# Optimization experiments

Hardware: AMD Instinct MI355X
Metric: run time of the kernel (lower is better)

The kernel has to match this reference:

```python
import jax, jax.numpy as jnp
import numpy as np

NEG = -1e9


def setup_inputs() -> dict:
    key = jax.random.key(0)
    kq, kk, kv, ke = jax.random.split(key, 4)
    B, H, S, D = 4, 16, 2048, 64
    q = jax.random.normal(kq, (B, H, S, D), dtype=jnp.float32)
    k = jax.random.normal(kk, (B, H, S, D), dtype=jnp.float32)
    v = jax.random.normal(kv, (B, H, S, D), dtype=jnp.float32)
    event_length = jax.random.randint(ke, (B,), 0, S, dtype=jnp.int32)
    return {"q": q, "k": k, "v": v, "event_length": event_length}


def reference(q, k, v, event_length):
    B, H, S, D = q.shape
    scale = jnp.sqrt(jnp.asarray(D, dtype=jnp.float32))
    # [b,h,s,q] scores
    scores = jnp.einsum('bhsd,bhqd->bhsq', q, k) / scale
    idx = jnp.arange(S)
    el = event_length[:, None]  # [B,1]
    valid = idx[None, :] < el   # [B,S]
    # mask[b,s,q] = valid[b,s] & valid[b,q]; broadcast over heads
    mask = (valid[:, None, :, None] & valid[:, None, None, :])  # [B,1,S,S]
    scores = jnp.where(mask, scores, NEG)
    attn = jax.nn.softmax(scores, axis=-1)
    # dropout p=0.0 (eval): identity
    out = jnp.einsum('bhsq,bhqd->bhsd', attn, v)
    return out
```

## Files before the change

### kernel.cpp

```cpp
#include <hip/hip_runtime.h>


#define SQ 2048
#define DH 64
#define NBH 64
#define TK 64
#define LDE 72

typedef __attribute__((ext_vector_type(4))) float f32x4;
typedef __attribute__((ext_vector_type(8))) short bf16x8;
typedef __attribute__((ext_vector_type(4))) unsigned int u32x4;
typedef __attribute__((ext_vector_type(2))) unsigned int u32x2;

__device__ __forceinline__ unsigned short bf16r(float x) {
    union { float f; unsigned int u; } t; t.f = x;
    unsigned int r = t.u + 0x7fffu + ((t.u >> 16) & 1u);
    return (unsigned short)(r >> 16);
}
__device__ __forceinline__ unsigned int bf16pk(float lo, float hi) {
    return (unsigned int)bf16r(lo) | ((unsigned int)bf16r(hi) << 16);
}

__global__ __launch_bounds__(256)
void meanv_k(const float* __restrict__ V, float* __restrict__ MV) {
    const int bh  = blockIdx.x >> 4;
    const int seg = blockIdx.x & 15;
    const float* vp = V + ((size_t)bh * SQ + (size_t)seg * 128) * DH;
    const int c = threadIdx.x & 15;
    const int r = threadIdx.x >> 4;
    const float* p = vp + (size_t)r * DH + c * 4;
    f32x4 s0 = *(const f32x4*)(p);
    f32x4 s1 = *(const f32x4*)(p + 16 * DH);
    f32x4 s2 = *(const f32x4*)(p + 32 * DH);
    f32x4 s3 = *(const f32x4*)(p + 48 * DH);
    s0 += *(const f32x4*)(p + 64 * DH);
    s1 += *(const f32x4*)(p + 80 * DH);
    s2 += *(const f32x4*)(p + 96 * DH);
    s3 += *(const f32x4*)(p + 112 * DH);
    f32x4 s = (s0 + s1) + (s2 + s3);
    __shared__ f32x4 red[16][16];
    red[r][c] = s;
    __syncthreads();
    if (threadIdx.x < 16) {
        f32x4 a = red[0][threadIdx.x];
        #pragma unroll
        for (int j = 1; j < 16; ++j) a += red[j][threadIdx.x];
        const float inv = 1.0f / (float)SQ;
        atomicAdd(&MV[bh * DH + threadIdx.x * 4 + 0], a[0] * inv);
        atomicAdd(&MV[bh * DH + threadIdx.x * 4 + 1], a[1] * inv);
        atomicAdd(&MV[bh * DH + threadIdx.x * 4 + 2], a[2] * inv);
        atomicAdd(&MV[bh * DH + threadIdx.x * 4 + 3], a[3] * inv);
    }
}

__global__ __launch_bounds__(256, 3)
void flash4(const float* __restrict__ Q, const float* __restrict__ K,
            const float* __restrict__ V, const int* __restrict__ EL,
            const float* __restrict__ MV, float* __restrict__ O) {
    const int bh    = blockIdx.x & (NBH - 1);
    const int qt    = blockIdx.x >> 6;
    const int el    = EL[bh >> 4];
    const int qbase = qt * 128;
    const int t     = threadIdx.x;

    const size_t base = (size_t)bh * SQ * DH;
    float* Op = O + base;

    if (qbase >= el) {
        const int c16 = t & 15, r0 = t >> 4;
        f32x4 mv = *(const f32x4*)(MV + bh * DH + c16 * 4);
        #pragma unroll
        for (int i = 0; i < 8; ++i)
            *(f32x4*)(Op + (size_t)(qbase + r0 + i * 16) * DH + c16 * 4) = mv;
        return;
    }

    const float* Qp = Q + base;
    const float* Kp = K + base;
    const float* Vp = V + base;

    const int wq = t >> 6, lane = t & 63, qd = lane >> 4, c = lane & 15;

    __shared__ short Kb[TK][LDE];
    __shared__ short Vt[DH][LDE];
    __shared__ short Pl[4][32][LDE];

    const float sc = 0.125f * 1.44269504f;
    bf16x8 qf[2][2];
    #pragma unroll
    for (int nt = 0; nt < 2; ++nt) {
        const int row = qbase + wq * 32 + nt * 16 + c;
        #pragma unroll
        for (int kc = 0; kc < 2; ++kc) {
            const float* p = Qp + (size_t)row * DH + kc * 32 + qd * 8;
            f32x4 a  = *(const f32x4*)p;
            f32x4 bb = *(const f32x4*)(p + 4);
            bf16x8 f;
            f[0] = (short)bf16r(a[0] * sc);  f[1] = (short)bf16r(a[1] * sc);
            f[2] = (short)bf16r(a[2] * sc);  f[3] = (short)bf16r(a[3] * sc);
            f[4] = (short)bf16r(bb[0] * sc); f[5] = (short)bf16r(bb[1] * sc);
            f[6] = (short)bf16r(bb[2] * sc); f[7] = (short)bf16r(bb[3] * sc);
            qf[nt][kc] = f;
        }
    }

    float l_[2] = {0.f, 0.f};
    f32x4 oacc[4][2];
    #pragma unroll
    for (int dt = 0; dt < 4; ++dt)
        #pragma unroll
        for (int nt = 0; nt < 2; ++nt)
            oacc[dt][nt] = (f32x4){0.f, 0.f, 0.f, 0.f};

    const int ksrow = t >> 2;
    const int ksdc  = t & 3;
    const int vpair = t & 31;
    const int vdg   = t >> 5;

    const int nkt = (el + TK - 1) / TK;

    f32x4 kg0, kg1, kg2, kg3, vg0, vg1, vg2, vg3;
    {
        const float* kp = Kp + (size_t)ksrow * DH + ksdc * 16;
        kg0 = *(const f32x4*)kp;
        kg1 = *(const f32x4*)(kp + 4);
        kg2 = *(const f32x4*)(kp + 8);
        kg3 = *(const f32x4*)(kp + 12);
        const float* vp0 = Vp + (size_t)(2 * vpair) * DH + vdg * 8;
        vg0 = *(const f32x4*)vp0;
        vg1 = *(const f32x4*)(vp0 + 4);
        vg2 = *(const f32x4*)(vp0 + DH);
        vg3 = *(const f32x4*)(vp0 + DH + 4);
    }

    for (int kt = 0; kt < nkt; ++kt) {
        const int k0 = kt * TK;

        __syncthreads();
        {
            u32x4 w0, w1;
            w0[0] = bf16pk(kg0[0], kg0[1]); w0[1] = bf16pk(kg0[2], kg0[3]);
            w0[2] = bf16pk(kg1[0], kg1[1]); w0[3] = bf16pk(kg1[2], kg1[3]);
            w1[0] = bf16pk(kg2[0], kg2[1]); w1[1] = bf16pk(kg2[2], kg2[3]);
            w1[2] = bf16pk(kg3[0], kg3[1]); w1[3] = bf16pk(kg3[2], kg3[3]);
            *(u32x4*)&Kb[ksrow][ksdc * 16]     = w0;
            *(u32x4*)&Kb[ksrow][ksdc * 16 + 8] = w1;
        }
        {
            #pragma unroll
            for (int i = 0; i < 4; ++i) {
                *(unsigned int*)&Vt[vdg * 8 + i][2 * vpair]     = bf16pk(vg0[i], vg2[i]);
                *(unsigned int*)&Vt[vdg * 8 + 4 + i][2 * vpair] = bf16pk(vg1[i], vg3[i]);
            }
        }
        __syncthreads();

        if (kt + 1 < nkt) {
            const int kn = k0 + TK;
            const float* kp = Kp + (size_t)(kn + ksrow) * DH + ksdc * 16;
            kg0 = *(const f32x4*)kp;
            kg1 = *(const f32x4*)(kp + 4);
            kg2 = *(const f32x4*)(kp + 8);
            kg3 = *(const f32x4*)(kp + 12);
            const float* vp0 = Vp + (size_t)(kn + 2 * vpair) * DH + vdg * 8;
            vg0 = *(const f32x4*)vp0;
            vg1 = *(const f32x4*)(vp0 + 4);
            vg2 = *(const f32x4*)(vp0 + DH);
            vg3 = *(const f32x4*)(vp0 + DH + 4);
        }

        f32x4 st[4][2];
        #pragma unroll
        for (int mt = 0; mt < 4; ++mt) {
            bf16x8 a0 = *(const bf16x8*)&Kb[mt * 16 + c][qd * 8];
            bf16x8 a1 = *(const bf16x8*)&Kb[mt * 16 + c][32 + qd * 8];
            #pragma unroll
            for (int nt = 0; nt < 2; ++nt) {
                f32x4 acc = (f32x4){0.f, 0.f, 0.f, 0.f};
                acc = __builtin_amdgcn_mfma_f32_16x16x32_bf16(a0, qf[nt][0], acc, 0, 0, 0);
                acc = __builtin_amdgcn_mfma_f32_16x16x32_bf16(a1, qf[nt][1], acc, 0, 0, 0);
                st[mt][nt] = acc;
            }
        }

        if (k0 + TK > el) {
            #pragma unroll
            for (int mt = 0; mt < 4; ++mt)
                #pragma unroll
                for (int r = 0; r < 4; ++r)
                    if (k0 + mt * 16 + qd * 4 + r >= el) {
                        st[mt][0][r] = -1e30f;
                        st[mt][1][r] = -1e30f;
                    }
        }

        #pragma unroll
        for (int nt = 0; nt < 2; ++nt) {
            #pragma unroll
            for (int mt = 0; mt < 4; ++mt) {
                const float p0 = exp2f(st[mt][nt][0]);
                const float p1 = exp2f(st[mt][nt][1]);
                const float p2 = exp2f(st[mt][nt][2]);
                const float p3 = exp2f(st[mt][nt][3]);
                l_[nt] += (p0 + p1) + (p2 + p3);
                u32x2 pw;
                pw[0] = bf16pk(p0, p1);
                pw[1] = bf16pk(p2, p3);
                *(u32x2*)&Pl[wq][nt * 16 + c][mt * 16 + qd * 4] = pw;
            }
        }

        #pragma unroll
        for (int kc = 0; kc < 2; ++kc) {
            bf16x8 pb0 = *(const bf16x8*)&Pl[wq][c][kc * 32 + qd * 8];
            bf16x8 pb1 = *(const bf16x8*)&Pl[wq][16 + c][kc * 32 + qd * 8];
            #pragma unroll
            for (int dt = 0; dt < 4; ++dt) {
                bf16x8 vf = *(const bf16x8*)&Vt[dt * 16 + c][kc * 32 + qd * 8];
                oacc[dt][0] = __builtin_amdgcn_mfma_f32_16x16x32_bf16(vf, pb0, oacc[dt][0], 0, 0, 0);
                oacc[dt][1] = __builtin_amdgcn_mfma_f32_16x16x32_bf16(vf, pb1, oacc[dt][1], 0, 0, 0);
            }
        }
    }

    #pragma unroll
    for (int nt = 0; nt < 2; ++nt) {
        l_[nt] += __shfl_xor(l_[nt], 16);
        l_[nt] += __shfl_xor(l_[nt], 32);
    }

    #pragma unroll
    for (int nt = 0; nt < 2; ++nt) {
        const int row = qbase + wq * 32 + nt * 16 + c;
        if (row < el) {
            const float inv = 1.0f / l_[nt];
            #pragma unroll
            for (int dt = 0; dt < 4; ++dt) {
                f32x4 o = oacc[dt][nt];
                o[0] *= inv; o[1] *= inv; o[2] *= inv; o[3] *= inv;
                *(f32x4*)(Op + (size_t)row * DH + dt * 16 + qd * 4) = o;
            }
        } else {
            #pragma unroll
            for (int dt = 0; dt < 4; ++dt) {
                f32x4 mv = *(const f32x4*)(MV + bh * DH + dt * 16 + qd * 4);
                *(f32x4*)(Op + (size_t)row * DH + dt * 16 + qd * 4) = mv;
            }
        }
    }
}

extern "C" void kernel_launch(void* const* d_in, const int* in_sizes, int n_in,
                              void* d_out, int out_size, void* d_ws, size_t ws_size,
                              hipStream_t stream) {
    const float* q  = (const float*)d_in[0];
    const float* k  = (const float*)d_in[1];
    const float* v  = (const float*)d_in[2];
    const int*   el = (const int*)d_in[3];
    float* out = (float*)d_out;
    float* mv  = (float*)d_ws;

    hipMemsetAsync(mv, 0, NBH * DH * sizeof(float), stream);
    meanv_k<<<dim3(NBH * 16), dim3(256), 0, stream>>>(v, mv);
    flash4<<<dim3(NBH * (SQ / 128)), dim3(256), 0, stream>>>(q, k, v, el, mv, out);
}
```

Baseline: 206.9 us.

## Schedule valid attention tiles via atomic work queue and use packed bf16 conversion

```diff
diff --git a/kernel.cpp b/kernel.cpp
--- a/kernel.cpp
+++ b/kernel.cpp
@@ -1,4 +1,5 @@
 #include <hip/hip_runtime.h>
+#include <hip/hip_bf16.h>
 
 
 #define SQ 2048
@@ -12,13 +13,10 @@
 typedef __attribute__((ext_vector_type(4))) unsigned int u32x4;
 typedef __attribute__((ext_vector_type(2))) unsigned int u32x2;
 
-__device__ __forceinline__ unsigned short bf16r(float x) {
-    union { float f; unsigned int u; } t; t.f = x;
-    unsigned int r = t.u + 0x7fffu + ((t.u >> 16) & 1u);
-    return (unsigned short)(r >> 16);
-}
-__device__ __forceinline__ unsigned int bf16pk(float lo, float hi) {
-    return (unsigned int)bf16r(lo) | ((unsigned int)bf16r(hi) << 16);
+__device__ __forceinline__ unsigned int pk2(float lo, float hi) {
+    __hip_bfloat162 h = __float22bfloat162_rn(float2{lo, hi});
+    union { __hip_bfloat162 h; unsigned int u; } c; c.h = h;
+    return c.u;
 }
 
 __global__ __launch_bounds__(256)
@@ -54,197 +52,222 @@
 }
 
 __global__ __launch_bounds__(256, 3)
-void flash4(const float* __restrict__ Q, const float* __restrict__ K,
+void flash5(const float* __restrict__ Q, const float* __restrict__ K,
             const float* __restrict__ V, const int* __restrict__ EL,
-            const float* __restrict__ MV, float* __restrict__ O) {
-    const int bh    = blockIdx.x & (NBH - 1);
-    const int qt    = blockIdx.x >> 6;
-    const int el    = EL[bh >> 4];
-    const int qbase = qt * 128;
-    const int t     = threadIdx.x;
-
-    const size_t base = (size_t)bh * SQ * DH;
-    float* Op = O + base;
-
-    if (qbase >= el) {
-        const int c16 = t & 15, r0 = t >> 4;
-        f32x4 mv = *(const f32x4*)(MV + bh * DH + c16 * 4);
-        #pragma unroll
-        for (int i = 0; i < 8; ++i)
-            *(f32x4*)(Op + (size_t)(qbase + r0 + i * 16) * DH + c16 * 4) = mv;
-        return;
+            const float* __restrict__ MV, float* __restrict__ O,
+            int* __restrict__ ticket) {
+    const int t = threadIdx.x;
+
+    {
+        const int bh0    = blockIdx.x & (NBH - 1);
+        const int qbase0 = (blockIdx.x >> 6) * 128;
+        const int el0    = EL[bh0 >> 4];
+        if (qbase0 >= el0) {
+            float* Op = O + (size_t)bh0 * SQ * DH;
+            const int c16 = t & 15, r0 = t >> 4;
+            f32x4 mv = *(const f32x4*)(MV + bh0 * DH + c16 * 4);
+            #pragma unroll
+            for (int i = 0; i < 8; ++i)
+                *(f32x4*)(Op + (size_t)(qbase0 + r0 + i * 16) * DH + c16 * 4) = mv;
+        }
     }
 
-    const float* Qp = Q + base;
-    const float* Kp = K + base;
-    const float* Vp = V + base;
-
-    const int wq = t >> 6, lane = t & 63, qd = lane >> 4, c = lane & 15;
+    const int el0 = EL[0], el1 = EL[1], el2 = EL[2], el3 = EL[3];
+    const int v0 = (el0 + 127) >> 7, v1 = (el1 + 127) >> 7;
+    const int v2 = (el2 + 127) >> 7, v3 = (el3 + 127) >> 7;
+    const int n0 = 16 * v0, n1 = n0 + 16 * v1, n2 = n1 + 16 * v2;
+    const int nvalid = n2 + 16 * v3;
 
     __shared__ short Kb[TK][LDE];
     __shared__ short Vt[DH][LDE];
     __shared__ short Pl[4][32][LDE];
-
-    const float sc = 0.125f * 1.44269504f;
-    bf16x8 qf[2][2];
-    #pragma unroll
-    for (int nt = 0; nt < 2; ++nt) {
-        const int row = qbase + wq * 32 + nt * 16 + c;
-        #pragma unroll
-        for (int kc = 0; kc < 2; ++kc) {
-            const float* p = Qp + (size_t)row * DH + kc * 32 + qd * 8;
-            f32x4 a  = *(const f32x4*)p;
-            f32x4 bb = *(const f32x4*)(p + 4);
-            bf16x8 f;
-            f[0] = (short)bf16r(a[0] * sc);  f[1] = (short)bf16r(a[1] * sc);
-            f[2] = (short)bf16r(a[2] * sc);  f[3] = (short)bf16r(a[3] * sc);
-            f[4] = (short)bf16r(bb[0] * sc); f[5] = (short)bf16r(bb[1] * sc);
-            f[6] = (short)bf16r(bb[2] * sc); f[7] = (short)bf16r(bb[3] * sc);
-            qf[nt][kc] = f;
-        }
-    }
-
-    float l_[2] = {0.f, 0.f};
-    f32x4 oacc[4][2];
-    #pragma unroll
-    for (int dt = 0; dt < 4; ++dt)
-        #pragma unroll
-        for (int nt = 0; nt < 2; ++nt)
-            oacc[dt][nt] = (f32x4){0.f, 0.f, 0.f, 0.f};
+    __shared__ int item_s;
+
+    const int wq = t >> 6, lane = t & 63, qd = lane >> 4, c = lane & 15;
 
     const int ksrow = t >> 2;
     const int ksdc  = t & 3;
     const int vpair = t & 31;
     const int vdg   = t >> 5;
 
-    const int nkt = (el + TK - 1) / TK;
-
-    f32x4 kg0, kg1, kg2, kg3, vg0, vg1, vg2, vg3;
-    {
-        const float* kp = Kp + (size_t)ksrow * DH + ksdc * 16;
-        kg0 = *(const f32x4*)kp;
-        kg1 = *(const f32x4*)(kp + 4);
-        kg2 = *(const f32x4*)(kp + 8);
-        kg3 = *(const f32x4*)(kp + 12);
-        const float* vp0 = Vp + (size_t)(2 * vpair) * DH + vdg * 8;
-        vg0 = *(const f32x4*)vp0;
-        vg1 = *(const f32x4*)(vp0 + 4);
-        vg2 = *(const f32x4*)(vp0 + DH);
-        vg3 = *(const f32x4*)(vp0 + DH + 4);
-    }
-
-    for (int kt = 0; kt < nkt; ++kt) {
-        const int k0 = kt * TK;
-
+    for (;;) {
+        if (t == 0) item_s = atomicAdd(ticket, 1);
         __syncthreads();
+        const int it = item_s;
+        if (it >= nvalid) break;
+
+        int b, u, vb, el;
+        if      (it < n0) { b = 0; u = it;      vb = v0; el = el0; }
+        else if (it < n1) { b = 1; u = it - n0; vb = v1; el = el1; }
+        else if (it < n2) { b = 2; u = it - n1; vb = v2; el = el2; }
+        else              { b = 3; u = it - n2; vb = v3; el = el3; }
+        const int head  = u / vb;
+        const int qt    = u - head * vb;
+        const int bh    = b * 16 + head;
+        const int qbase = qt * 128;
+
+        const size_t base = (size_t)bh * SQ * DH;
+        const float* Qp = Q + base;
+        const float* Kp = K + base;
+        const float* Vp = V + base;
+        float* Op = O + base;
+
+        const float sc = 0.125f * 1.44269504f;
+        bf16x8 qf[2][2];
+        #pragma unroll
+        for (int nt = 0; nt < 2; ++nt) {
+            const int row = qbase + wq * 32 + nt * 16 + c;
+            #pragma unroll
+            for (int kc = 0; kc < 2; ++kc) {
+                const float* p = Qp + (size_t)row * DH + kc * 32 + qd * 8;
+                f32x4 a  = *(const f32x4*)p;
+                f32x4 bb = *(const f32x4*)(p + 4);
+                u32x4 f;
+                f[0] = pk2(a[0] * sc, a[1] * sc);
+                f[1] = pk2(a[2] * sc, a[3] * sc);
+                f[2] = pk2(bb[0] * sc, bb[1] * sc);
+                f[3] = pk2(bb[2] * sc, bb[3] * sc);
+                qf[nt][kc] = *(bf16x8*)&f;
+            }
+        }
+
+        float l_[2] = {0.f, 0.f};
+        f32x4 oacc[4][2];
+        #pragma unroll
+        for (int dt = 0; dt < 4; ++dt)
+            #pragma unroll
+            for (int nt = 0; nt < 2; ++nt)
+                oacc[dt][nt] = (f32x4){0.f, 0.f, 0.f, 0.f};
+
+        const int nkt = (el + TK - 1) / TK;
+
+        f32x4 kg0, kg1, kg2, kg3, vg0, vg1, vg2, vg3;
         {
-            u32x4 w0, w1;
-            w0[0] = bf16pk(kg0[0], kg0[1]); w0[1] = bf16pk(kg0[2], kg0[3]);
-            w0[2] = bf16pk(kg1[0], kg1[1]); w0[3] = bf16pk(kg1[2], kg1[3]);
-            w1[0] = bf16pk(kg2[0], kg2[1]); w1[1] = bf16pk(kg2[2], kg2[3]);
-            w1[2] = bf16pk(kg3[0], kg3[1]); w1[3] = bf16pk(kg3[2], kg3[3]);
-            *(u32x4*)&Kb[ksrow][ksdc * 16]     = w0;
-            *(u32x4*)&Kb[ksrow][ksdc * 16 + 8] = w1;
-        }
-        {
-            #pragma unroll
-            for (int i = 0; i < 4; ++i) {
-                *(unsigned int*)&Vt[vdg * 8 + i][2 * vpair]     = bf16pk(vg0[i], vg2[i]);
-                *(unsigned int*)&Vt[vdg * 8 + 4 + i][2 * vpair] = bf16pk(vg1[i], vg3[i]);
-            }
-        }
-        __syncthreads();
-
-        if (kt + 1 < nkt) {
-            const int kn = k0 + TK;
-            const float* kp = Kp + (size_t)(kn + ksrow) * DH + ksdc * 16;
+            const float* kp = Kp + (size_t)ksrow * DH + ksdc * 16;
             kg0 = *(const f32x4*)kp;
             kg1 = *(const f32x4*)(kp + 4);
             kg2 = *(const f32x4*)(kp + 8);
             kg3 = *(const f32x4*)(kp + 12);
-            const float* vp0 = Vp + (size_t)(kn + 2 * vpair) * DH + vdg * 8;
+            const float* vp0 = Vp + (size_t)(2 * vpair) * DH + vdg * 8;
             vg0 = *(const f32x4*)vp0;
             vg1 = *(const f32x4*)(vp0 + 4);
             vg2 = *(const f32x4*)(vp0 + DH);
             vg3 = *(const f32x4*)(vp0 + DH + 4);
         }
 
-        f32x4 st[4][2];
-        #pragma unroll
-        for (int mt = 0; mt < 4; ++mt) {
-            bf16x8 a0 = *(const bf16x8*)&Kb[mt * 16 + c][qd * 8];
-            bf16x8 a1 = *(const bf16x8*)&Kb[mt * 16 + c][32 + qd * 8];
+        for (int kt = 0; kt < nkt; ++kt) {
+            const int k0 = kt * TK;
+
+            __syncthreads();
+            {
+                u32x4 w0, w1;
+                w0[0] = pk2(kg0[0], kg0[1]); w0[1] = pk2(kg0[2], kg0[3]);
+                w0[2] = pk2(kg1[0], kg1[1]); w0[3] = pk2(kg1[2], kg1[3]);
+                w1[0] = pk2(kg2[0], kg2[1]); w1[1] = pk2(kg2[2], kg2[3]);
+                w1[2] = pk2(kg3[0], kg3[1]); w1[3] = pk2(kg3[2], kg3[3]);
+                *(u32x4*)&Kb[ksrow][ksdc * 16]     = w0;
+                *(u32x4*)&Kb[ksrow][ksdc * 16 + 8] = w1;
+            }
+            {
+                #pragma unroll
+                for (int i = 0; i < 4; ++i) {
+                    *(unsigned int*)&Vt[vdg * 8 + i][2 * vpair]     = pk2(vg0[i], vg2[i]);
+                    *(unsigned int*)&Vt[vdg * 8 + 4 + i][2 * vpair] = pk2(vg1[i], vg3[i]);
+                }
+            }
+            __syncthreads();
+
+            if (kt + 1 < nkt) {
+                const int kn = k0 + TK;
+                const float* kp = Kp + (size_t)(kn + ksrow) * DH + ksdc * 16;
+                kg0 = *(const f32x4*)kp;
+                kg1 = *(const f32x4*)(kp + 4);
+                kg2 = *(const f32x4*)(kp + 8);
+                kg3 = *(const f32x4*)(kp + 12);
+                const float* vp0 = Vp + (size_t)(kn + 2 * vpair) * DH + vdg * 8;
+                vg0 = *(const f32x4*)vp0;
+                vg1 = *(const f32x4*)(vp0 + 4);
+                vg2 = *(const f32x4*)(vp0 + DH);
+                vg3 = *(const f32x4*)(vp0 + DH + 4);
+            }
+
+            f32x4 st[4][2];
+            #pragma unroll
+            for (int mt = 0; mt < 4; ++mt) {
+                bf16x8 a0 = *(const bf16x8*)&Kb[mt * 16 + c][qd * 8];
+                bf16x8 a1 = *(const bf16x8*)&Kb[mt * 16 + c][32 + qd * 8];
+                #pragma unroll
+                for (int nt = 0; nt < 2; ++nt) {
+                    f32x4 acc = (f32x4){0.f, 0.f, 0.f, 0.f};
+                    acc = __builtin_amdgcn_mfma_f32_16x16x32_bf16(a0, qf[nt][0], acc, 0, 0, 0);
+                    acc = __builtin_amdgcn_mfma_f32_16x16x32_bf16(a1, qf[nt][1], acc, 0, 0, 0);
+                    st[mt][nt] = acc;
+                }
+            }
+
+            if (k0 + TK > el) {
+                #pragma unroll
+                for (int mt = 0; mt < 4; ++mt)
+                    #pragma unroll
+                    for (int r = 0; r < 4; ++r)
+                        if (k0 + mt * 16 + qd * 4 + r >= el) {
+                            st[mt][0][r] = -1e30f;
+                            st[mt][1][r] = -1e30f;
+                        }
+            }
+
             #pragma unroll
             for (int nt = 0; nt < 2; ++nt) {
-                f32x4 acc = (f32x4){0.f, 0.f, 0.f, 0.f};
-                acc = __builtin_amdgcn_mfma_f32_16x16x32_bf16(a0, qf[nt][0], acc, 0, 0, 0);
-                acc = __builtin_amdgcn_mfma_f32_16x16x32_bf16(a1, qf[nt][1], acc, 0, 0, 0);
-                st[mt][nt] = acc;
-            }
-        }
-
-        if (k0 + TK > el) {
-            #pragma unroll
-            for (int mt = 0; mt < 4; ++mt)
-                #pragma unroll
-                for (int r = 0; r < 4; ++r)
-                    if (k0 + mt * 16 + qd * 4 + r >= el) {
-                        st[mt][0][r] = -1e30f;
-                        st[mt][1][r] = -1e30f;
-                    }
+                #pragma unroll
+                for (int mt = 0; mt < 4; ++mt) {
+                    const float p0 = exp2f(st[mt][nt][0]);
+                    const float p1 = exp2f(st[mt][nt][1]);
+                    const float p2 = exp2f(st[mt][nt][2]);
+                    const float p3 = exp2f(st[mt][nt][3]);
+                    l_[nt] += (p0 + p1) + (p2 + p3);
+                    u32x2 pw;
+                    pw[0] = pk2(p0, p1);
+                    pw[1] = pk2(p2, p3);
+                    *(u32x2*)&Pl[wq][nt * 16 + c][mt * 16 + qd * 4] = pw;
+                }
+            }
+
+            #pragma unroll
+            for (int kc = 0; kc < 2; ++kc) {
+                bf16x8 pb0 = *(const bf16x8*)&Pl[wq][c][kc * 32 + qd * 8];
+                bf16x8 pb1 = *(const bf16x8*)&Pl[wq][16 + c][kc * 32 + qd * 8];
+                #pragma unroll
+                for (int dt = 0; dt < 4; ++dt) {
+                    bf16x8 vf = *(const bf16x8*)&Vt[dt * 16 + c][kc * 32 + qd * 8];
+                    oacc[dt][0] = __builtin_amdgcn_mfma_f32_16x16x32_bf16(vf, pb0, oacc[dt][0], 0, 0, 0);
+                    oacc[dt][1] = __builtin_amdgcn_mfma_f32_16x16x32_bf16(vf, pb1, oacc[dt][1], 0, 0, 0);
+                }
+            }
         }
 
         #pragma unroll
         for (int nt = 0; nt < 2; ++nt) {
-            #pragma unroll
-            for (int mt = 0; mt < 4; ++mt) {
-                const float p0 = exp2f(st[mt][nt][0]);
-                const float p1 = exp2f(st[mt][nt][1]);
-                const float p2 = exp2f(st[mt][nt][2]);
-                const float p3 = exp2f(st[mt][nt][3]);
-                l_[nt] += (p0 + p1) + (p2 + p3);
-                u32x2 pw;
-                pw[0] = bf16pk(p0, p1);
-                pw[1] = bf16pk(p2, p3);
-                *(u32x2*)&Pl[wq][nt * 16 + c][mt * 16 + qd * 4] = pw;
-            }
-        }
-
-        #pragma unroll
-        for (int kc = 0; kc < 2; ++kc) {
-            bf16x8 pb0 = *(const bf16x8*)&Pl[wq][c][kc * 32 + qd * 8];
-            bf16x8 pb1 = *(const bf16x8*)&Pl[wq][16 + c][kc * 32 + qd * 8];
-            #pragma unroll
-            for (int dt = 0; dt < 4; ++dt) {
-                bf16x8 vf = *(const bf16x8*)&Vt[dt * 16 + c][kc * 32 + qd * 8];
-                oacc[dt][0] = __builtin_amdgcn_mfma_f32_16x16x32_bf16(vf, pb0, oacc[dt][0], 0, 0, 0);
-                oacc[dt][1] = __builtin_amdgcn_mfma_f32_16x16x32_bf16(vf, pb1, oacc[dt][1], 0, 0, 0);
-            }
-        }
-    }
-
-    #pragma unroll
-    for (int nt = 0; nt < 2; ++nt) {
-        l_[nt] += __shfl_xor(l_[nt], 16);
-        l_[nt] += __shfl_xor(l_[nt], 32);
-    }
-
-    #pragma unroll
-    for (int nt = 0; nt < 2; ++nt) {
-        const int row = qbase + wq * 32 + nt * 16 + c;
-        if (row < el) {
-            const float inv = 1.0f / l_[nt];
-            #pragma unroll
-            for (int dt = 0; dt < 4; ++dt) {
-                f32x4 o = oacc[dt][nt];
-                o[0] *= inv; o[1] *= inv; o[2] *= inv; o[3] *= inv;
-                *(f32x4*)(Op + (size_t)row * DH + dt * 16 + qd * 4) = o;
-            }
-        } else {
-            #pragma unroll
-            for (int dt = 0; dt < 4; ++dt) {
-                f32x4 mv = *(const f32x4*)(MV + bh * DH + dt * 16 + qd * 4);
-                *(f32x4*)(Op + (size_t)row * DH + dt * 16 + qd * 4) = mv;
+            l_[nt] += __shfl_xor(l_[nt], 16);
+            l_[nt] += __shfl_xor(l_[nt], 32);
+        }
+
+        #pragma unroll
+        for (int nt = 0; nt < 2; ++nt) {
+            const int row = qbase + wq * 32 + nt * 16 + c;
+            if (row < el) {
+                const float inv = 1.0f / l_[nt];
+                #pragma unroll
+                for (int dt = 0; dt < 4; ++dt) {
+                    f32x4 o = oacc[dt][nt];
+                    o[0] *= inv; o[1] *= inv; o[2] *= inv; o[3] *= inv;
+                    *(f32x4*)(Op + (size_t)row * DH + dt * 16 + qd * 4) = o;
+                }
+            } else {
+                #pragma unroll
+                for (int dt = 0; dt < 4; ++dt) {
+                    f32x4 mv = *(const f32x4*)(MV + bh * DH + dt * 16 + qd * 4);
+                    *(f32x4*)(Op + (size_t)row * DH + dt * 16 + qd * 4) = mv;
+                }
             }
         }
     }
@@ -259,8 +282,9 @@
     const int*   el = (const int*)d_in[3];
     float* out = (float*)d_out;
     float* mv  = (float*)d_ws;
-
-    hipMemsetAsync(mv, 0, NBH * DH * sizeof(float), stream);
+    int*   tk  = (int*)((char*)d_ws + NBH * DH * sizeof(float));
+
+    hipMemsetAsync(d_ws, 0, NBH * DH * sizeof(float) + 64, stream);
     meanv_k<<<dim3(NBH * 16), dim3(256), 0, stream>>>(v, mv);
-    flash4<<<dim3(NBH * (SQ / 128)), dim3(256), 0, stream>>>(q, k, v, el, mv, out);
-}
+    flash5<<<dim3(NBH * (SQ / 128)), dim3(256), 0, stream>>>(q, k, v, el, mv, out, tk);
+}
```

Measured after the change: 203.3 us. About the same (-1.7%).
